# Kernel tuning notes

Hardware: AMD Instinct MI355X
Metric: run time of the kernel (lower is better)

Reference implementation:

```python
import jax, jax.numpy as jnp
import numpy as np

NUM_TAGS = 128
SEQ_LEN = 256
BATCH = 512
PAD_IDX = -1  # Padding.WORD_LABEL_PAD_IDX


def setup_inputs() -> dict:
    key = jax.random.key(0)
    k1, k2, k3 = jax.random.split(key, 3)
    T = NUM_TAGS
    emissions = jax.random.normal(k1, (SEQ_LEN, BATCH, T), dtype=jnp.float32)
    tags = jax.random.randint(k2, (SEQ_LEN, BATCH), 0, T, dtype=jnp.int32)
    # transitions param: uniform(-0.1, 0.1), never transition INTO start, never FROM end
    transitions = jax.random.uniform(k3, (T + 2, T + 2), minval=-0.1, maxval=0.1, dtype=jnp.float32)
    transitions = transitions.at[:, T].set(-10000.0)      # start_tag column
    transitions = transitions.at[T + 1, :].set(-10000.0)  # end_tag row
    return {"emissions": emissions, "transitions": transitions, "tags": tags}


def reference(emissions, transitions, tags):
    T = transitions.shape[0] - 2
    start_tag, end_tag = T, T + 1
    S, B = tags.shape
    mask = (tags != PAD_IDX).astype(emissions.dtype)  # (S, B)

    # ---- numerator: joint log-likelihood of gold path ----
    # per-timestep gold emission scores, (S, B)
    emit = jnp.take_along_axis(emissions, tags[:, :, None], axis=2)[..., 0]
    llh = transitions[start_tag, tags[0]]                              # start transition
    llh = llh + jnp.sum(emit[:-1] * mask[:-1], axis=0)                 # emissions for t in [0, S-1)
    llh = llh + jnp.sum(transitions[tags[:-1], tags[1:]] * mask[1:], axis=0)  # transitions
    last_idx = mask.sum(axis=0).astype(jnp.int32) - 1                  # (B,)
    last_tags = tags[last_idx, jnp.arange(B)]
    llh = llh + transitions[last_tags, end_tag]
    llh = llh + emissions[-1, jnp.arange(B), last_tags] * mask[-1]

    # ---- denominator: log partition via forward algorithm (scan over time) ----
    trans_tt = transitions[:T, :T]                                      # (T, T)
    log_prob0 = transitions[start_tag, :T][None, :] + emissions[0]      # (B, T)

    def step(log_prob, inp):
        e, m = inp  # e: (B, T), m: (B,)
        # score[b, j] = logsumexp_i(log_prob[b, i] + trans[i, j] + e[b, j])
        score = jax.nn.logsumexp(log_prob[:, :, None] + trans_tt[None, :, :] + e[:, None, :], axis=1)
        log_prob = jnp.where(m[:, None] > 0, score, log_prob)
        return log_prob, None

    log_prob, _ = jax.lax.scan(step, log_prob0, (emissions[1:], mask[1:]))
    denom = jax.nn.logsumexp(log_prob + transitions[:T, end_tag][None, :], axis=1)  # (B,)

    return jnp.mean(llh - denom)  # reduce=True
```

## Files before the change

kernel.cpp:

```cpp
#include <hip/hip_runtime.h>

#define S_LEN 256
#define B_SZ  512
#define T_TAGS 128
#define TP2   130
#define PAD_I (-1)
#define RS    4

#define FWD_BLOCKS 32
#define NQ 32
#define QLEN 8
#define NUM_SUB 4
#define NUM_BLOCKS (NQ * NUM_SUB)
#define TOT_BLOCKS (FWD_BLOCKS + NUM_BLOCKS)

typedef __bf16 bf16x8 __attribute__((ext_vector_type(8)));
typedef float  f32x4  __attribute__((ext_vector_type(4)));

#define PI_J(c, lg, e) ((2*(c) + ((e) >> 2))*16 + (lg)*4 + ((e) & 3))

__device__ __forceinline__ void bar_lds() {
    asm volatile("s_waitcnt lgkmcnt(0)\n\ts_barrier" ::: "memory");
}

__device__ __forceinline__ void consumer_step(
    int s, int buf,
    const bf16x8 (&A)[8][4], bf16x8 (&Q)[4], float &M, int &tgc,
    const int* __restrict__ tags, int b0, int l, int lm,
    const float (&EE)[2][8][64][4])
{
    const int sn  = (s + 1 < S_LEN) ? s + 1 : S_LEN - 1;
    const int tgn = tags[sn * B_SZ + b0 + lm];

    f32x4 d[8];
    const f32x4 z = {0.f, 0.f, 0.f, 0.f};
    #pragma unroll
    for (int jt = 0; jt < 8; ++jt) {
        d[jt] = __builtin_amdgcn_mfma_f32_16x16x32_bf16(A[jt][0], Q[0], z, 0, 0, 0);
        #pragma unroll
        for (int c = 1; c < 4; ++c)
            d[jt] = __builtin_amdgcn_mfma_f32_16x16x32_bf16(A[jt][c], Q[c], d[jt], 0, 0, 0);
    }
    float u[8][4];
    #pragma unroll
    for (int jt = 0; jt < 8; ++jt) {
        const f32x4 ee = *(const f32x4*)&EE[buf][jt][l][0];
        #pragma unroll
        for (int r = 0; r < 4; ++r) u[jt][r] = d[jt][r] * ee[r];
    }
    float Mn = M;
    if ((s & (RS - 1)) == 0) {
        float R = u[0][0];
        #pragma unroll
        for (int jt = 0; jt < 8; ++jt)
            #pragma unroll
            for (int r = 0; r < 4; ++r) R = fmaxf(R, u[jt][r]);
        R = fmaxf(R, __shfl_xor(R, 16));
        R = fmaxf(R, __shfl_xor(R, 32));
        const float rr = 1.0f / R;
        Mn = M + __logf(R);
        #pragma unroll
        for (int jt = 0; jt < 8; ++jt)
            #pragma unroll
            for (int r = 0; r < 4; ++r) u[jt][r] *= rr;
    }
    bf16x8 Qn[4];
    #pragma unroll
    for (int c = 0; c < 4; ++c)
        #pragma unroll
        for (int e = 0; e < 8; ++e)
            Qn[c][e] = (__bf16)u[2*c + (e >> 2)][e & 3];
    const bool live = (tgc != PAD_I);
    M = live ? Mn : M;
    #pragma unroll
    for (int c = 0; c < 4; ++c) Q[c] = live ? Qn[c] : Q[c];
    tgc = tgn;
}

__global__ __launch_bounds__(192) void crf_main(
    const float* __restrict__ em,
    const float* __restrict__ trans,
    const int*   __restrict__ tags,
    float* __restrict__ denom_out,
    float* __restrict__ pl,
    int*   __restrict__ pc)
{
    const int t = threadIdx.x;
    if (blockIdx.x < FWD_BLOCKS) {
        const int w  = t >> 6;
        const int l  = t & 63;
        const int lm = l & 15;
        const int lg = l >> 4;
        const int b0 = blockIdx.x * 16;

        __shared__ __align__(16) float EE[2][8][64][4];

        if (w == 0) {
            bf16x8 A[8][4];
            #pragma unroll
            for (int jt = 0; jt < 8; ++jt)
                #pragma unroll
                for (int c = 0; c < 4; ++c)
                    #pragma unroll
                    for (int e = 0; e < 8; ++e)
                        A[jt][c][e] = (__bf16)__expf(trans[PI_J(c, lg, e)*TP2 + jt*16 + lm]);

            f32x4 em0[8];
            #pragma unroll
            for (int jt = 0; jt < 8; ++jt)
                em0[jt] = *(const f32x4*)&em[((size_t)0*B_SZ + b0 + lm)*T_TAGS + jt*16 + lg*4];
            bf16x8 Q[4];
            #pragma unroll
            for (int c = 0; c < 4; ++c)
                #pragma unroll
                for (int e = 0; e < 8; ++e) {
                    const int j  = PI_J(c, lg, e);
                    const int jt = 2*c + (e >> 2);
                    const int r  = e & 3;
                    Q[c][e] = (__bf16)__expf(trans[T_TAGS*TP2 + j] + em0[jt][r]);
                }
            float M = 0.f;
            int tgc = tags[1*B_SZ + b0 + lm];
            bar_lds();

            for (int i = 1; i < S_LEN - 1; i += 2) {
                consumer_step(i,     1, A, Q, M, tgc, tags, b0, l, lm, EE);
                bar_lds();
                consumer_step(i + 1, 0, A, Q, M, tgc, tags, b0, l, lm, EE);
                bar_lds();
            }
            consumer_step(S_LEN - 1, 1, A, Q, M, tgc, tags, b0, l, lm, EE);

            float sum = 0.f;
            #pragma unroll
            for (int c = 0; c < 4; ++c)
                #pragma unroll
                for (int e = 0; e < 8; ++e)
                    sum += (float)Q[c][e] * __expf(trans[PI_J(c, lg, e)*TP2 + (T_TAGS + 1)]);
            sum += __shfl_xor(sum, 16);
            sum += __shfl_xor(sum, 32);
            if (l < 16)
                denom_out[b0 + l] = M + __logf(sum);
        } else {
            const int pjt0 = (w - 1) * 4;
            f32x4 pA[4], pB[4];
            #pragma unroll
            for (int q = 0; q < 4; ++q)
                pA[q] = *(const f32x4*)&em[((size_t)1*B_SZ + b0 + lm)*T_TAGS + (pjt0 + q)*16 + lg*4];
            #pragma unroll
            for (int q = 0; q < 4; ++q) {
                f32x4 v;
                #pragma unroll
                for (int r = 0; r < 4; ++r) v[r] = __expf(pA[q][r]);
                *(f32x4*)&EE[1][pjt0 + q][l][0] = v;
            }
            #pragma unroll
            for (int q = 0; q < 4; ++q)
                pB[q] = *(const f32x4*)&em[((size_t)2*B_SZ + b0 + lm)*T_TAGS + (pjt0 + q)*16 + lg*4];
            bar_lds();

            for (int i = 1; i < S_LEN - 1; i += 2) {
                #pragma unroll
                for (int q = 0; q < 4; ++q) {
                    f32x4 v;
                    #pragma unroll
                    for (int r = 0; r < 4; ++r) v[r] = __expf(pB[q][r]);
                    *(f32x4*)&EE[0][pjt0 + q][l][0] = v;
                }
                #pragma unroll
                for (int q = 0; q < 4; ++q)
                    pA[q] = *(const f32x4*)&em[((size_t)(i + 2)*B_SZ + b0 + lm)*T_TAGS + (pjt0 + q)*16 + lg*4];
                bar_lds();
                #pragma unroll
                for (int q = 0; q < 4; ++q) {
                    f32x4 v;
                    #pragma unroll
                    for (int r = 0; r < 4; ++r) v[r] = __expf(pA[q][r]);
                    *(f32x4*)&EE[1][pjt0 + q][l][0] = v;
                }
                const int s3 = (i + 3 < S_LEN) ? i + 3 : S_LEN - 1;
                #pragma unroll
                for (int q = 0; q < 4; ++q)
                    pB[q] = *(const f32x4*)&em[((size_t)s3*B_SZ + b0 + lm)*T_TAGS + (pjt0 + q)*16 + lg*4];
                bar_lds();
            }
        }
    } else {
        if (t >= 128) return;
        const int nb = blockIdx.x - FWD_BLOCKS;
        const int q  = nb >> 2;
        const int b  = (nb & 3) * 128 + t;
        const int s0 = q * QLEN;

        int tg[QLEN + 1];
        tg[0] = (s0 == 0) ? PAD_I : tags[(s0 - 1)*B_SZ + b];
        #pragma unroll
        for (int k = 0; k < QLEN; ++k)
            tg[k + 1] = tags[(s0 + k)*B_SZ + b];

        float acc = 0.f;
        int cnt = 0;
        if (q == 0) {
            const int t0  = tg[1];
            const int t0w = (t0 < 0) ? t0 + TP2 : t0;
            acc += trans[T_TAGS*TP2 + t0w];
        }
        #pragma unroll
        for (int k = 0; k < QLEN; ++k) {
            const int s = s0 + k;
            const int c = tg[k + 1];
            const float m = (c != PAD_I) ? 1.f : 0.f;
            cnt += (c != PAD_I) ? 1 : 0;
            if (s >= 1) {
                const int p  = tg[k];
                const int pw = (p < 0) ? p + TP2 : p;
                const int cw = (c < 0) ? c + TP2 : c;
                acc += trans[pw*TP2 + cw] * m;
            }
            if (s <= S_LEN - 2) {
                int cc = c; if (cc < 0) cc = 0;
                acc += em[((size_t)s*B_SZ + b)*T_TAGS + cc] * m;
            }
        }
        pl[q*B_SZ + b] = acc;
        pc[q*B_SZ + b] = cnt;
    }
}

__global__ __launch_bounds__(64) void finish_kernel(
    const float* __restrict__ em,
    const float* __restrict__ trans,
    const int*   __restrict__ tags,
    const float* __restrict__ pl, const int* __restrict__ pc,
    const float* __restrict__ denom,
    float* __restrict__ out)
{
    const int b = blockIdx.x * 64 + threadIdx.x;
    float llh = 0.f;
    int cnt = 0;
    #pragma unroll
    for (int q = 0; q < NQ; ++q) {
        llh += pl[q*B_SZ + b];
        cnt += pc[q*B_SZ + b];
    }
    int li = cnt - 1; if (li < 0) li = 0;
    const int lt  = tags[li*B_SZ + b];
    const int ltw = (lt < 0) ? lt + TP2 : lt;
    llh += trans[ltw*TP2 + (T_TAGS + 1)];
    const float ml = (tags[(S_LEN - 1)*B_SZ + b] != PAD_I) ? 1.f : 0.f;
    int ltc = lt; if (ltc < 0) ltc = 0;
    llh += em[((size_t)(S_LEN - 1)*B_SZ + b)*T_TAGS + ltc] * ml;

    float v = llh - denom[b];
    #pragma unroll
    for (int off = 32; off; off >>= 1)
        v += __shfl_xor(v, off);
    if (threadIdx.x == 0)
        atomicAdd(out, v * (1.f / (float)B_SZ));
}

extern "C" void kernel_launch(void* const* d_in, const int* in_sizes, int n_in,
                              void* d_out, int out_size, void* d_ws, size_t ws_size,
                              hipStream_t stream) {
    const float* em    = (const float*)d_in[0];
    const float* trans = (const float*)d_in[1];
    const int*   tags  = (const int*)d_in[2];
    float* out   = (float*)d_out;

    float* denom = (float*)d_ws;
    float* pl    = denom + B_SZ;
    int*   pc    = (int*)(pl + NQ*B_SZ);

    hipMemsetAsync(d_out, 0, sizeof(float), stream);
    crf_main<<<TOT_BLOCKS, 192, 0, stream>>>(em, trans, tags, denom, pl, pc);
    finish_kernel<<<B_SZ / 64, 64, 0, stream>>>(em, trans, tags, pl, pc, denom, out);
}
```

Before: 220.5 us.

## Deepen emission exp pipeline to four LDS slots and fuse finish into main kernel

Grows the shared exp(emission) ring buffer from two to four slots so producer waves run two steps ahead. The consumer now needs only one barrier per timestep and prefetches tags two steps ahead, which takes global tag loads off the recurrence critical path. The separate finish kernel is replaced by a last-block-done reduction that uses an atomic counter, which removes one kernel launch. This adds fences and an atomic per block, and enlarges the LDS footprint for every block.

```diff
diff --git a/kernel.cpp b/kernel.cpp
--- a/kernel.cpp
+++ b/kernel.cpp
@@ -13,6 +13,7 @@
 #define NUM_SUB 4
 #define NUM_BLOCKS (NQ * NUM_SUB)
 #define TOT_BLOCKS (FWD_BLOCKS + NUM_BLOCKS)
+#define NTHR 192
 
 typedef __bf16 bf16x8 __attribute__((ext_vector_type(8)));
 typedef float  f32x4  __attribute__((ext_vector_type(4)));
@@ -24,14 +25,9 @@
 }
 
 __device__ __forceinline__ void consumer_step(
-    int s, int buf,
-    const bf16x8 (&A)[8][4], bf16x8 (&Q)[4], float &M, int &tgc,
-    const int* __restrict__ tags, int b0, int l, int lm,
-    const float (&EE)[2][8][64][4])
+    int s, const bf16x8 (&A)[8][4], bf16x8 (&Q)[4], float &M, int tgc,
+    const float (&EE)[4][8][64][4], int l)
 {
-    const int sn  = (s + 1 < S_LEN) ? s + 1 : S_LEN - 1;
-    const int tgn = tags[sn * B_SZ + b0 + lm];
-
     f32x4 d[8];
     const f32x4 z = {0.f, 0.f, 0.f, 0.f};
     #pragma unroll
@@ -44,7 +40,7 @@
     float u[8][4];
     #pragma unroll
     for (int jt = 0; jt < 8; ++jt) {
-        const f32x4 ee = *(const f32x4*)&EE[buf][jt][l][0];
+        const f32x4 ee = *(const f32x4*)&EE[s & 3][jt][l][0];
         #pragma unroll
         for (int r = 0; r < 4; ++r) u[jt][r] = d[jt][r] * ee[r];
     }
@@ -74,18 +70,22 @@
     M = live ? Mn : M;
     #pragma unroll
     for (int c = 0; c < 4; ++c) Q[c] = live ? Qn[c] : Q[c];
-    tgc = tgn;
-}
-
-__global__ __launch_bounds__(192) void crf_main(
+}
+
+__global__ __launch_bounds__(NTHR) void crf_main(
     const float* __restrict__ em,
     const float* __restrict__ trans,
     const int*   __restrict__ tags,
     float* __restrict__ denom_out,
     float* __restrict__ pl,
-    int*   __restrict__ pc)
+    int*   __restrict__ pc,
+    unsigned int* __restrict__ counter,
+    float* __restrict__ out)
 {
+    __shared__ __align__(16) float EE[4][8][64][4];
+    __shared__ int lastflag;
     const int t = threadIdx.x;
+
     if (blockIdx.x < FWD_BLOCKS) {
         const int w  = t >> 6;
         const int l  = t & 63;
@@ -93,8 +93,6 @@
         const int lg = l >> 4;
         const int b0 = blockIdx.x * 16;
 
-        __shared__ __align__(16) float EE[2][8][64][4];
-
         if (w == 0) {
             bf16x8 A[8][4];
             #pragma unroll
@@ -120,16 +118,18 @@
                     Q[c][e] = (__bf16)__expf(trans[T_TAGS*TP2 + j] + em0[jt][r]);
                 }
             float M = 0.f;
-            int tgc = tags[1*B_SZ + b0 + lm];
+            int tg_cur = tags[1*B_SZ + b0 + lm];
+            int tg_nxt = tags[2*B_SZ + b0 + lm];
             bar_lds();
 
-            for (int i = 1; i < S_LEN - 1; i += 2) {
-                consumer_step(i,     1, A, Q, M, tgc, tags, b0, l, lm, EE);
+            for (int s = 1; s <= S_LEN - 2; ++s) {
+                const int sf = (s + 2 < S_LEN) ? s + 2 : S_LEN - 1;
+                const int tg_fut = tags[sf*B_SZ + b0 + lm];
+                consumer_step(s, A, Q, M, tg_cur, EE, l);
+                tg_cur = tg_nxt; tg_nxt = tg_fut;
                 bar_lds();
-                consumer_step(i + 1, 0, A, Q, M, tgc, tags, b0, l, lm, EE);
-                bar_lds();
-            }
-            consumer_step(S_LEN - 1, 1, A, Q, M, tgc, tags, b0, l, lm, EE);
+            }
+            consumer_step(S_LEN - 1, A, Q, M, tg_cur, EE, l);
 
             float sum = 0.f;
             #pragma unroll
@@ -142,121 +142,113 @@
             if (l < 16)
                 denom_out[b0 + l] = M + __logf(sum);
         } else {
-            const int pjt0 = (w - 1) * 4;
-            f32x4 pA[4], pB[4];
-            #pragma unroll
-            for (int q = 0; q < 4; ++q)
-                pA[q] = *(const f32x4*)&em[((size_t)1*B_SZ + b0 + lm)*T_TAGS + (pjt0 + q)*16 + lg*4];
-            #pragma unroll
-            for (int q = 0; q < 4; ++q) {
-                f32x4 v;
-                #pragma unroll
-                for (int r = 0; r < 4; ++r) v[r] = __expf(pA[q][r]);
-                *(f32x4*)&EE[1][pjt0 + q][l][0] = v;
-            }
-            #pragma unroll
-            for (int q = 0; q < 4; ++q)
-                pB[q] = *(const f32x4*)&em[((size_t)2*B_SZ + b0 + lm)*T_TAGS + (pjt0 + q)*16 + lg*4];
-            bar_lds();
-
-            for (int i = 1; i < S_LEN - 1; i += 2) {
+            const int pj = (w - 1) * 4;
+            auto LOADV = [&](f32x4 (&dst)[4], int s) {
+                #pragma unroll
+                for (int q = 0; q < 4; ++q)
+                    dst[q] = *(const f32x4*)&em[((size_t)s*B_SZ + b0 + lm)*T_TAGS + (pj + q)*16 + lg*4];
+            };
+            auto EXPW = [&](int slot, const f32x4 (&src)[4]) {
                 #pragma unroll
                 for (int q = 0; q < 4; ++q) {
                     f32x4 v;
                     #pragma unroll
-                    for (int r = 0; r < 4; ++r) v[r] = __expf(pB[q][r]);
-                    *(f32x4*)&EE[0][pjt0 + q][l][0] = v;
-                }
-                #pragma unroll
-                for (int q = 0; q < 4; ++q)
-                    pA[q] = *(const f32x4*)&em[((size_t)(i + 2)*B_SZ + b0 + lm)*T_TAGS + (pjt0 + q)*16 + lg*4];
+                    for (int r = 0; r < 4; ++r) v[r] = __expf(src[q][r]);
+                    *(f32x4*)&EE[slot][pj + q][l][0] = v;
+                }
+            };
+            f32x4 t0[4], t1[4], sA[4], sB[4];
+            LOADV(t0, 1); LOADV(t1, 2);
+            EXPW(1, t0);  EXPW(2, t1);
+            LOADV(sB, 3); LOADV(sA, 4);
+            bar_lds();
+
+            for (int i = 1; i <= 253; i += 2) {
+                EXPW((i + 2) & 3, sB);
+                { const int s4 = (i + 4 < S_LEN) ? i + 4 : S_LEN - 1; LOADV(sB, s4); }
                 bar_lds();
-                #pragma unroll
-                for (int q = 0; q < 4; ++q) {
-                    f32x4 v;
-                    #pragma unroll
-                    for (int r = 0; r < 4; ++r) v[r] = __expf(pA[q][r]);
-                    *(f32x4*)&EE[1][pjt0 + q][l][0] = v;
-                }
-                const int s3 = (i + 3 < S_LEN) ? i + 3 : S_LEN - 1;
-                #pragma unroll
-                for (int q = 0; q < 4; ++q)
-                    pB[q] = *(const f32x4*)&em[((size_t)s3*B_SZ + b0 + lm)*T_TAGS + (pjt0 + q)*16 + lg*4];
+                EXPW((i + 3) & 3, sA);
+                { const int s5 = (i + 5 < S_LEN) ? i + 5 : S_LEN - 1; LOADV(sA, s5); }
                 bar_lds();
             }
         }
     } else {
-        if (t >= 128) return;
-        const int nb = blockIdx.x - FWD_BLOCKS;
-        const int q  = nb >> 2;
-        const int b  = (nb & 3) * 128 + t;
-        const int s0 = q * QLEN;
-
-        int tg[QLEN + 1];
-        tg[0] = (s0 == 0) ? PAD_I : tags[(s0 - 1)*B_SZ + b];
-        #pragma unroll
-        for (int k = 0; k < QLEN; ++k)
-            tg[k + 1] = tags[(s0 + k)*B_SZ + b];
-
-        float acc = 0.f;
-        int cnt = 0;
-        if (q == 0) {
-            const int t0  = tg[1];
-            const int t0w = (t0 < 0) ? t0 + TP2 : t0;
-            acc += trans[T_TAGS*TP2 + t0w];
+        if (t < 128) {
+            const int nb = blockIdx.x - FWD_BLOCKS;
+            const int q  = nb >> 2;
+            const int b  = (nb & 3) * 128 + t;
+            const int s0 = q * QLEN;
+
+            int tg[QLEN + 1];
+            tg[0] = (s0 == 0) ? PAD_I : tags[(s0 - 1)*B_SZ + b];
+            #pragma unroll
+            for (int k = 0; k < QLEN; ++k)
+                tg[k + 1] = tags[(s0 + k)*B_SZ + b];
+
+            float acc = 0.f;
+            int cnt = 0;
+            if (q == 0) {
+                const int t0  = tg[1];
+                const int t0w = (t0 < 0) ? t0 + TP2 : t0;
+                acc += trans[T_TAGS*TP2 + t0w];
+            }
+            #pragma unroll
+            for (int k = 0; k < QLEN; ++k) {
+                const int s = s0 + k;
+                const int c = tg[k + 1];
+                const float m = (c != PAD_I) ? 1.f : 0.f;
+                cnt += (c != PAD_I) ? 1 : 0;
+                if (s >= 1) {
+                    const int p  = tg[k];
+                    const int pw = (p < 0) ? p + TP2 : p;
+                    const int cw = (c < 0) ? c + TP2 : c;
+                    acc += trans[pw*TP2 + cw] * m;
+                }
+                if (s <= S_LEN - 2) {
+                    int cc = c; if (cc < 0) cc = 0;
+                    acc += em[((size_t)s*B_SZ + b)*T_TAGS + cc] * m;
+                }
+            }
+            pl[q*B_SZ + b] = acc;
+            pc[q*B_SZ + b] = cnt;
         }
-        #pragma unroll
-        for (int k = 0; k < QLEN; ++k) {
-            const int s = s0 + k;
-            const int c = tg[k + 1];
-            const float m = (c != PAD_I) ? 1.f : 0.f;
-            cnt += (c != PAD_I) ? 1 : 0;
-            if (s >= 1) {
-                const int p  = tg[k];
-                const int pw = (p < 0) ? p + TP2 : p;
-                const int cw = (c < 0) ? c + TP2 : c;
-                acc += trans[pw*TP2 + cw] * m;
-            }
-            if (s <= S_LEN - 2) {
-                int cc = c; if (cc < 0) cc = 0;
-                acc += em[((size_t)s*B_SZ + b)*T_TAGS + cc] * m;
-            }
+    }
+
+    __threadfence();
+    if (t == 0) {
+        const unsigned old = atomicAdd(counter, 1u);
+        lastflag = (old == TOT_BLOCKS - 1) ? 1 : 0;
+    }
+    __syncthreads();
+    if (lastflag) {
+        __threadfence();
+        float part = 0.f;
+        for (int b = t; b < B_SZ; b += NTHR) {
+            float llh = 0.f;
+            int cnt = 0;
+            #pragma unroll
+            for (int q = 0; q < NQ; ++q) {
+                llh += pl[q*B_SZ + b];
+                cnt += pc[q*B_SZ + b];
+            }
+            int li = cnt - 1; if (li < 0) li = 0;
+            const int lt  = tags[li*B_SZ + b];
+            const int ltw = (lt < 0) ? lt + TP2 : lt;
+            llh += trans[ltw*TP2 + (T_TAGS + 1)];
+            const float ml = (tags[(S_LEN - 1)*B_SZ + b] != PAD_I) ? 1.f : 0.f;
+            int ltc = lt; if (ltc < 0) ltc = 0;
+            llh += em[((size_t)(S_LEN - 1)*B_SZ + b)*T_TAGS + ltc] * ml;
+            part += llh - denom_out[b];
         }
-        pl[q*B_SZ + b] = acc;
-        pc[q*B_SZ + b] = cnt;
-    }
-}
-
-__global__ __launch_bounds__(64) void finish_kernel(
-    const float* __restrict__ em,
-    const float* __restrict__ trans,
-    const int*   __restrict__ tags,
-    const float* __restrict__ pl, const int* __restrict__ pc,
-    const float* __restrict__ denom,
-    float* __restrict__ out)
-{
-    const int b = blockIdx.x * 64 + threadIdx.x;
-    float llh = 0.f;
-    int cnt = 0;
-    #pragma unroll
-    for (int q = 0; q < NQ; ++q) {
-        llh += pl[q*B_SZ + b];
-        cnt += pc[q*B_SZ + b];
-    }
-    int li = cnt - 1; if (li < 0) li = 0;
-    const int lt  = tags[li*B_SZ + b];
-    const int ltw = (lt < 0) ? lt + TP2 : lt;
-    llh += trans[ltw*TP2 + (T_TAGS + 1)];
-    const float ml = (tags[(S_LEN - 1)*B_SZ + b] != PAD_I) ? 1.f : 0.f;
-    int ltc = lt; if (ltc < 0) ltc = 0;
-    llh += em[((size_t)(S_LEN - 1)*B_SZ + b)*T_TAGS + ltc] * ml;
-
-    float v = llh - denom[b];
-    #pragma unroll
-    for (int off = 32; off; off >>= 1)
-        v += __shfl_xor(v, off);
-    if (threadIdx.x == 0)
-        atomicAdd(out, v * (1.f / (float)B_SZ));
+        #pragma unroll
+        for (int off = 32; off; off >>= 1)
+            part += __shfl_xor(part, off);
+        float* red = &EE[0][0][0][0];
+        if ((t & 63) == 0) red[t >> 6] = part;
+        __syncthreads();
+        if (t == 0)
+            out[0] = (red[0] + red[1] + red[2]) * (1.f / (float)B_SZ);
+    }
 }
 
 extern "C" void kernel_launch(void* const* d_in, const int* in_sizes, int n_in,
@@ -270,8 +262,8 @@
     float* denom = (float*)d_ws;
     float* pl    = denom + B_SZ;
     int*   pc    = (int*)(pl + NQ*B_SZ);
-
-    hipMemsetAsync(d_out, 0, sizeof(float), stream);
-    crf_main<<<TOT_BLOCKS, 192, 0, stream>>>(em, trans, tags, denom, pl, pc);
-    finish_kernel<<<B_SZ / 64, 64, 0, stream>>>(em, trans, tags, pl, pc, denom, out);
-}
+    unsigned int* counter = (unsigned int*)(pc + NQ*B_SZ);
+
+    hipMemsetAsync(counter, 0, sizeof(unsigned int), stream);
+    crf_main<<<TOT_BLOCKS, NTHR, 0, stream>>>(em, trans, tags, denom, pl, pc, counter, out);
+}
```

Measured after the change: 248.4 us. 12.7% more time.
